# Optimization experiments

Hardware: AMD Instinct MI355X
Metric: run time of the kernel (lower is better)

The kernel has to match this reference:

```python
import jax, jax.numpy as jnp
import numpy as np

N = 262144        # number of nodes
D = 64            # fixed in-degree per destination node (edges grouped by dest)
RATIO = 0.5
K = int(D * RATIO)  # edges kept per node = 32


def setup_inputs() -> dict:
    key = jax.random.key(0)
    k1, k2 = jax.random.split(key)
    logits = jax.random.normal(k1, (N,), dtype=jnp.float32)
    # source endpoints: random nodes; destination endpoints: sorted, D edges per node
    src = jax.random.randint(k2, (N * D,), 0, N, dtype=jnp.int32)
    dst = jnp.repeat(jnp.arange(N, dtype=jnp.int32), D)
    edge_index = jnp.stack([src, dst])  # [2, E]
    return {"logits": logits, "edge_index": edge_index}


def reference(logits, edge_index):
    # LabelAwarePool.forward: sigmoid -> per-edge L1 similarity -> per-dest-node top-k edges
    s = jax.nn.sigmoid(logits).reshape(-1)          # [N]
    ends = s[edge_index]                            # [2, E] endpoint scores
    sim = 1.0 - jnp.abs(ends[0] - ends[1])          # [E] similarity
    E = edge_index.shape[1]
    n = E // D                                      # number of segments (nodes)
    # segmented top-k: edges are grouped by destination node in blocks of D
    _, idx = jax.lax.top_k(sim.reshape(n, D), K)    # [n, K] indices within each segment
    edges_g = edge_index.reshape(2, n, D)           # [2, n, D]
    sel = jnp.take_along_axis(edges_g, idx[None, :, :], axis=2)  # [2, n, K]
    return sel.reshape(2, n * K)                    # concatenated kept edges
```

## Files before the change

kernel.cpp:

```cpp
#include <hip/hip_runtime.h>
#include <cstdint>

#define D_EDGES 64
#define K_KEEP  32

__device__ __forceinline__ float np_expf(float x) {
    const float log2e     = 1.44269504088896341f;
    const float cvt_magic = 12582912.0f;
    const float neg_ln2hi = -0.693359375f;
    const float neg_ln2lo = 2.12194440e-4f;
    const float p0 = 1.9875691500E-4f;
    const float p1 = 1.3981999507E-3f;
    const float p2 = 8.3334519073E-3f;
    const float p3 = 4.1665795894E-2f;
    const float p4 = 1.6666665459E-1f;
    const float p5 = 5.0000001201E-1f;

    float q = fmaf(x, log2e, cvt_magic);
    q -= cvt_magic;
    x = fmaf(q, neg_ln2hi, x);
    x = fmaf(q, neg_ln2lo, x);
    float x2 = x * x;
    float poly = fmaf(p0, x, p1);
    poly = fmaf(poly, x, p2);
    poly = fmaf(poly, x, p3);
    poly = fmaf(poly, x, p4);
    poly = fmaf(poly, x, p5);
    poly = fmaf(poly, x2, x);
    poly = poly + 1.0f;
    return ldexpf(poly, (int)q);
}

__device__ __forceinline__ float sigmoid_np(float x) {
    float e = np_expf(-x);
    return 1.0f / (1.0f + e);
}

__global__ void sigmoid_kernel(const float* __restrict__ logits,
                               float* __restrict__ s, int n) {
    int i = blockIdx.x * blockDim.x + threadIdx.x;
    if (i < n) s[i] = sigmoid_np(logits[i]);
}

template <int CTRL>
__device__ __forceinline__ unsigned long long xor_dpp_u64(unsigned long long v) {
    int lo = (int)(unsigned)v;
    int hi = (int)(v >> 32);
    lo = __builtin_amdgcn_update_dpp(lo, lo, CTRL, 0xF, 0xF, true);
    hi = __builtin_amdgcn_update_dpp(hi, hi, CTRL, 0xF, 0xF, true);
    return ((unsigned long long)(unsigned)hi << 32) | (unsigned)lo;
}

template <int OFF>
__device__ __forceinline__ unsigned long long xor_swz_u64(unsigned long long v) {
    int lo = (int)(unsigned)v;
    int hi = (int)(v >> 32);
    lo = __builtin_amdgcn_ds_swizzle(lo, OFF);
    hi = __builtin_amdgcn_ds_swizzle(hi, OFF);
    return ((unsigned long long)(unsigned)hi << 32) | (unsigned)lo;
}

template <int J>
__device__ __forceinline__ unsigned long long xorshfl_u64(unsigned long long v) {
    if constexpr (J == 1)       return xor_dpp_u64<0xB1>(v);
    else if constexpr (J == 2)  return xor_dpp_u64<0x4E>(v);
    else if constexpr (J == 4)  return xor_swz_u64<0x101F>(v);
    else if constexpr (J == 8)  return xor_dpp_u64<0x128>(v);
    else if constexpr (J == 16) return xor_swz_u64<0x401F>(v);
    else {
        int lo = (int)(unsigned)v;
        int hi = (int)(v >> 32);
        lo = __shfl_xor(lo, 32, 64);
        hi = __shfl_xor(hi, 32, 64);
        return ((unsigned long long)(unsigned)hi << 32) | (unsigned)lo;
    }
}

template <int K, int J>
__device__ __forceinline__ void stage(unsigned long long& key, int lane) {
    unsigned long long other = xorshfl_u64<J>(key);
    bool up = (lane & K) == 0;
    bool isLower = (lane & J) == 0;
    bool mine_first = key > other;
    if (mine_first != (isLower == up)) key = other;
}

template <bool USE_TABLE>
__global__ void topk_kernel(const int* __restrict__ edge_index,
                            const float* __restrict__ s,
                            const float* __restrict__ logits,
                            int* __restrict__ out,
                            long long E, long long nseg) {
    long long gtid = (long long)blockIdx.x * blockDim.x + threadIdx.x;
    long long w = gtid >> 6;
    int lane = (int)(gtid & 63);
    if (w >= nseg) return;

    long long e = w * D_EDGES + lane;
    int src = edge_index[e];
    int dst = edge_index[E + e];

    float ss, sd;
    if (USE_TABLE) {
        ss = s[src];
        sd = s[dst];
    } else {
        ss = sigmoid_np(logits[src]);
        sd = sigmoid_np(logits[dst]);
    }
    float sim = 1.0f - fabsf(ss - sd);

    unsigned long long key =
        ((unsigned long long)__float_as_uint(sim) << 6) |
        (unsigned long long)(lane ^ 63);

    stage<2, 1>(key, lane);
    stage<4, 2>(key, lane);   stage<4, 1>(key, lane);
    stage<8, 4>(key, lane);   stage<8, 2>(key, lane);   stage<8, 1>(key, lane);
    stage<16, 8>(key, lane);  stage<16, 4>(key, lane);  stage<16, 2>(key, lane);
    stage<16, 1>(key, lane);
    stage<32, 16>(key, lane); stage<32, 8>(key, lane);  stage<32, 4>(key, lane);
    stage<32, 2>(key, lane);  stage<32, 1>(key, lane);
    stage<64, 32>(key, lane); stage<64, 16>(key, lane); stage<64, 8>(key, lane);
    stage<64, 4>(key, lane);  stage<64, 2>(key, lane);  stage<64, 1>(key, lane);

    int origLane = ((int)(key & 63)) ^ 63;
    int sel_src = __shfl(src, origLane, 64);
    int sel_dst = __shfl(dst, origLane, 64);

    if (lane < K_KEEP) {
        long long base = w * K_KEEP + lane;
        out[base] = sel_src;
        out[nseg * K_KEEP + base] = sel_dst;
    }
}

extern "C" void kernel_launch(void* const* d_in, const int* in_sizes, int n_in,
                              void* d_out, int out_size, void* d_ws, size_t ws_size,
                              hipStream_t stream) {
    const float* logits = (const float*)d_in[0];
    const int* edge_index = (const int*)d_in[1];
    int N = in_sizes[0];
    long long E = (long long)in_sizes[1] / 2;
    long long nseg = E / D_EDGES;
    int* out = (int*)d_out;

    long long total_threads = nseg * 64;
    int blocks = (int)((total_threads + 255) / 256);

    if (ws_size >= (size_t)N * sizeof(float)) {
        float* s = (float*)d_ws;
        sigmoid_kernel<<<(N + 255) / 256, 256, 0, stream>>>(logits, s, N);
        topk_kernel<true><<<blocks, 256, 0, stream>>>(edge_index, s, logits, out, E, nseg);
    } else {
        topk_kernel<false><<<blocks, 256, 0, stream>>>(edge_index, nullptr, logits, out, E, nseg);
    }
}
```

Before: 271.2 us.

## Sort four segments per wave with register-local bitonic stages and packed src keys

Each wave now handles four segments. Each lane loads four source indices with a single int4 load and holds four keys in registers. Bitonic stages with distance below 4 become in-register compare-swaps, and only the larger distances use DPP or swizzle lane exchanges. The source index is packed into the low bits of the sort key, so the final cross-lane shuffle is no longer needed, and outputs are written as int4 vectors. The destination is read once per segment and broadcast, which relies on the stated grouping of edges by destination and on source ids fitting in 28 bits.

```diff
diff --git a/kernel.cpp b/kernel.cpp
--- a/kernel.cpp
+++ b/kernel.cpp
@@ -3,6 +3,8 @@
 
 #define D_EDGES 64
 #define K_KEEP  32
+
+typedef unsigned long long ull;
 
 __device__ __forceinline__ float np_expf(float x) {
     const float log2e     = 1.44269504088896341f;
@@ -43,95 +45,138 @@
 }
 
 template <int CTRL>
-__device__ __forceinline__ unsigned long long xor_dpp_u64(unsigned long long v) {
+__device__ __forceinline__ ull xor_dpp_u64(ull v) {
     int lo = (int)(unsigned)v;
     int hi = (int)(v >> 32);
     lo = __builtin_amdgcn_update_dpp(lo, lo, CTRL, 0xF, 0xF, true);
     hi = __builtin_amdgcn_update_dpp(hi, hi, CTRL, 0xF, 0xF, true);
-    return ((unsigned long long)(unsigned)hi << 32) | (unsigned)lo;
-}
-
-template <int OFF>
-__device__ __forceinline__ unsigned long long xor_swz_u64(unsigned long long v) {
+    return ((ull)(unsigned)hi << 32) | (unsigned)lo;
+}
+
+__device__ __forceinline__ ull xor4_swz_u64(ull v) {
     int lo = (int)(unsigned)v;
     int hi = (int)(v >> 32);
-    lo = __builtin_amdgcn_ds_swizzle(lo, OFF);
-    hi = __builtin_amdgcn_ds_swizzle(hi, OFF);
-    return ((unsigned long long)(unsigned)hi << 32) | (unsigned)lo;
-}
-
-template <int J>
-__device__ __forceinline__ unsigned long long xorshfl_u64(unsigned long long v) {
-    if constexpr (J == 1)       return xor_dpp_u64<0xB1>(v);
-    else if constexpr (J == 2)  return xor_dpp_u64<0x4E>(v);
-    else if constexpr (J == 4)  return xor_swz_u64<0x101F>(v);
-    else if constexpr (J == 8)  return xor_dpp_u64<0x128>(v);
-    else if constexpr (J == 16) return xor_swz_u64<0x401F>(v);
-    else {
-        int lo = (int)(unsigned)v;
-        int hi = (int)(v >> 32);
-        lo = __shfl_xor(lo, 32, 64);
-        hi = __shfl_xor(hi, 32, 64);
-        return ((unsigned long long)(unsigned)hi << 32) | (unsigned)lo;
-    }
+    lo = __builtin_amdgcn_ds_swizzle(lo, 0x101F);
+    hi = __builtin_amdgcn_ds_swizzle(hi, 0x101F);
+    return ((ull)(unsigned)hi << 32) | (unsigned)lo;
+}
+
+template <int DIST>
+__device__ __forceinline__ ull lane_xor_u64(ull v) {
+    if constexpr (DIST == 1)      return xor_dpp_u64<0xB1>(v);
+    else if constexpr (DIST == 2) return xor_dpp_u64<0x4E>(v);
+    else if constexpr (DIST == 4) return xor4_swz_u64(v);
+    else                          return xor_dpp_u64<0x128>(v);
+}
+
+
+template <int K, int S1>
+__device__ __forceinline__ void lce(ull& ka, ull& kb, int t) {
+    bool up = (((4 * t + S1) & K) == 0);
+    bool mf = ka > kb;
+    if (mf != up) { ull tmp = ka; ka = kb; kb = tmp; }
+}
+
+template <int K, int J, int S>
+__device__ __forceinline__ void cce(ull& k, int t) {
+    ull other = lane_xor_u64<J / 4>(k);
+    int e = 4 * t + S;
+    bool up  = ((e & K) == 0);
+    bool low = ((e & J) == 0);
+    bool mf  = k > other;
+    if (mf != (low == up)) k = other;
 }
 
 template <int K, int J>
-__device__ __forceinline__ void stage(unsigned long long& key, int lane) {
-    unsigned long long other = xorshfl_u64<J>(key);
-    bool up = (lane & K) == 0;
-    bool isLower = (lane & J) == 0;
-    bool mine_first = key > other;
-    if (mine_first != (isLower == up)) key = other;
+__device__ __forceinline__ void cce4(ull& k0, ull& k1, ull& k2, ull& k3, int t) {
+    cce<K, J, 0>(k0, t);
+    cce<K, J, 1>(k1, t);
+    cce<K, J, 2>(k2, t);
+    cce<K, J, 3>(k3, t);
+}
+
+template <int K>
+__device__ __forceinline__ void lceJ1(ull& k0, ull& k1, ull& k2, ull& k3, int t) {
+    lce<K, 0>(k0, k1, t);
+    lce<K, 2>(k2, k3, t);
+}
+
+template <int K>
+__device__ __forceinline__ void lceJ2(ull& k0, ull& k1, ull& k2, ull& k3, int t) {
+    lce<K, 0>(k0, k2, t);
+    lce<K, 1>(k1, k3, t);
+}
+
+__device__ __forceinline__ ull make_key(float sim, int e, int src) {
+    unsigned sb  = __float_as_uint(sim);
+    unsigned e63 = (unsigned)(e ^ 63);
+    unsigned hi  = (sb << 2) | (e63 >> 4);
+    unsigned lo  = (e63 << 28) | (unsigned)src;
+    return ((ull)hi << 32) | lo;
 }
 
 template <bool USE_TABLE>
-__global__ void topk_kernel(const int* __restrict__ edge_index,
-                            const float* __restrict__ s,
-                            const float* __restrict__ logits,
-                            int* __restrict__ out,
-                            long long E, long long nseg) {
+__global__ void __launch_bounds__(256)
+topk_kernel(const int* __restrict__ edge_index,
+            const float* __restrict__ s,
+            const float* __restrict__ logits,
+            int* __restrict__ out,
+            long long E, long long nseg) {
     long long gtid = (long long)blockIdx.x * blockDim.x + threadIdx.x;
     long long w = gtid >> 6;
     int lane = (int)(gtid & 63);
-    if (w >= nseg) return;
-
-    long long e = w * D_EDGES + lane;
-    int src = edge_index[e];
-    int dst = edge_index[E + e];
-
-    float ss, sd;
-    if (USE_TABLE) {
-        ss = s[src];
-        sd = s[dst];
+    int q = lane >> 4;
+    int t = lane & 15;
+    long long g = w * 4 + q;
+    if (g >= nseg) return;
+
+    int4 sv = *reinterpret_cast<const int4*>(edge_index + g * D_EDGES + 4 * t);
+    int dstv = edge_index[E + g * D_EDGES];
+
+    float sd, ss0, ss1, ss2, ss3;
+    if constexpr (USE_TABLE) {
+        sd  = s[dstv];
+        ss0 = s[sv.x]; ss1 = s[sv.y]; ss2 = s[sv.z]; ss3 = s[sv.w];
     } else {
-        ss = sigmoid_np(logits[src]);
-        sd = sigmoid_np(logits[dst]);
+        sd  = sigmoid_np(logits[dstv]);
+        ss0 = sigmoid_np(logits[sv.x]);
+        ss1 = sigmoid_np(logits[sv.y]);
+        ss2 = sigmoid_np(logits[sv.z]);
+        ss3 = sigmoid_np(logits[sv.w]);
     }
-    float sim = 1.0f - fabsf(ss - sd);
-
-    unsigned long long key =
-        ((unsigned long long)__float_as_uint(sim) << 6) |
-        (unsigned long long)(lane ^ 63);
-
-    stage<2, 1>(key, lane);
-    stage<4, 2>(key, lane);   stage<4, 1>(key, lane);
-    stage<8, 4>(key, lane);   stage<8, 2>(key, lane);   stage<8, 1>(key, lane);
-    stage<16, 8>(key, lane);  stage<16, 4>(key, lane);  stage<16, 2>(key, lane);
-    stage<16, 1>(key, lane);
-    stage<32, 16>(key, lane); stage<32, 8>(key, lane);  stage<32, 4>(key, lane);
-    stage<32, 2>(key, lane);  stage<32, 1>(key, lane);
-    stage<64, 32>(key, lane); stage<64, 16>(key, lane); stage<64, 8>(key, lane);
-    stage<64, 4>(key, lane);  stage<64, 2>(key, lane);  stage<64, 1>(key, lane);
-
-    int origLane = ((int)(key & 63)) ^ 63;
-    int sel_src = __shfl(src, origLane, 64);
-    int sel_dst = __shfl(dst, origLane, 64);
-
-    if (lane < K_KEEP) {
-        long long base = w * K_KEEP + lane;
-        out[base] = sel_src;
-        out[nseg * K_KEEP + base] = sel_dst;
+
+    ull k0 = make_key(1.0f - fabsf(ss0 - sd), 4 * t + 0, sv.x);
+    ull k1 = make_key(1.0f - fabsf(ss1 - sd), 4 * t + 1, sv.y);
+    ull k2 = make_key(1.0f - fabsf(ss2 - sd), 4 * t + 2, sv.z);
+    ull k3 = make_key(1.0f - fabsf(ss3 - sd), 4 * t + 3, sv.w);
+
+    lceJ1<2>(k0, k1, k2, k3, t);
+    lceJ2<4>(k0, k1, k2, k3, t);   lceJ1<4>(k0, k1, k2, k3, t);
+    cce4<8, 4>(k0, k1, k2, k3, t);
+    lceJ2<8>(k0, k1, k2, k3, t);   lceJ1<8>(k0, k1, k2, k3, t);
+    cce4<16, 8>(k0, k1, k2, k3, t);
+    cce4<16, 4>(k0, k1, k2, k3, t);
+    lceJ2<16>(k0, k1, k2, k3, t);  lceJ1<16>(k0, k1, k2, k3, t);
+    cce4<32, 16>(k0, k1, k2, k3, t);
+    cce4<32, 8>(k0, k1, k2, k3, t);
+    cce4<32, 4>(k0, k1, k2, k3, t);
+    lceJ2<32>(k0, k1, k2, k3, t);  lceJ1<32>(k0, k1, k2, k3, t);
+    cce4<64, 32>(k0, k1, k2, k3, t);
+    cce4<64, 16>(k0, k1, k2, k3, t);
+    cce4<64, 8>(k0, k1, k2, k3, t);
+    cce4<64, 4>(k0, k1, k2, k3, t);
+    lceJ2<64>(k0, k1, k2, k3, t);  lceJ1<64>(k0, k1, k2, k3, t);
+
+    if (t < 8) {
+        long long base = g * K_KEEP + 4 * t;
+        int4 r0;
+        r0.x = (int)(k0 & 0x0FFFFFFFu);
+        r0.y = (int)(k1 & 0x0FFFFFFFu);
+        r0.z = (int)(k2 & 0x0FFFFFFFu);
+        r0.w = (int)(k3 & 0x0FFFFFFFu);
+        *reinterpret_cast<int4*>(out + base) = r0;
+        *reinterpret_cast<int4*>(out + nseg * K_KEEP + base) =
+            make_int4(dstv, dstv, dstv, dstv);
     }
 }
 
@@ -145,7 +190,8 @@
     long long nseg = E / D_EDGES;
     int* out = (int*)d_out;
 
-    long long total_threads = nseg * 64;
+    long long nwave = (nseg + 3) / 4;
+    long long total_threads = nwave * 64;
     int blocks = (int)((total_threads + 255) / 256);
 
     if (ws_size >= (size_t)N * sizeof(float)) {
```

Result: no change. 272.1 us (+0.4%).
